# Kernel tuning notes

Hardware: AMD Instinct MI355X
Metric: run time of the kernel (lower is better)

## Reference

```python
import jax, jax.numpy as jnp
import numpy as np

S = 16   # num_states
C = 8    # input_channels
B = 64   # batch
L = 4096 # sequence length


def hyperbolic_sigmoid(x):
    return x / (1 + jnp.abs(x)) * 0.5 + 0.5


def hyperbolic_softmax(logits, axis):
    x = hyperbolic_sigmoid(logits)
    return x / jnp.sum(x, axis=axis, keepdims=True)


def setup_inputs() -> dict:
    key = jax.random.key(0)
    k0, k1, k2, k3 = jax.random.split(key, 4)
    return {
        "log_input_probs": jax.random.normal(k0, (B, L, C), dtype=jnp.float32),
        "invh_initial_state_probs": jax.random.normal(k1, (S,), dtype=jnp.float32),
        "invh_transition_probs": jax.random.normal(k2, (S, C, S), dtype=jnp.float32),
        "invh_accepting_state_probs": jax.random.normal(k3, (S,), dtype=jnp.float32),
    }


def reference(log_input_probs, invh_initial_state_probs, invh_transition_probs, invh_accepting_state_probs):
    # hyperbolic parameterization -> probabilities
    initial_state_probs = hyperbolic_softmax(invh_initial_state_probs, axis=0)         # (S,)
    transition_probs = hyperbolic_softmax(invh_transition_probs, axis=2)               # (S,C,S)
    accepting_state_logprobs = jnp.log(hyperbolic_sigmoid(invh_accepting_state_probs)) # (S,)

    input_probs = jnp.exp(log_input_probs)  # (B,L,C)
    # per-timestep transition matrices, (B,L,S,S)
    trans_each = jnp.einsum('pcn,blc->blpn', transition_probs, input_probs)
    # log-depth chain product m0 @ m1 @ ... @ m_{L-1} via associative scan
    prefix = jax.lax.associative_scan(jnp.matmul, trans_each, axis=1)
    transition_overall = prefix[:, -1]  # (B,S,S)
    # p_state[b,n] = sum_p overall[b,p,n] * init[p]
    p_state = jnp.einsum('bpn,p->bn', transition_overall, initial_state_probs)
    log_p_state = jnp.log(p_state + 1e-20)
    log_acceptance = jax.nn.logsumexp(log_p_state + accepting_state_logprobs[None, :], axis=1)  # (B,)
    return log_acceptance[None]  # (1,B)
```

## Files before the change

kernel.cpp:

```cpp
#include <hip/hip_runtime.h>
#include <math.h>

#define S 16
#define C 8
#define NB 64
#define L 4096
#define K 64
#define LC 64

#define SLOT 324
#define RS 20

typedef __attribute__((ext_vector_type(8))) short bf16x8;
typedef __attribute__((ext_vector_type(4))) short bf16x4;
typedef __attribute__((ext_vector_type(4))) float f32x4;
typedef unsigned long long ull;

#define WS_INIT 0
#define WS_ACC  64
#define WS_CLOG 512
#define WS_TTT  16896
#define WS_CP   49664

__device__ __forceinline__ float hsig(float x) {
    return x / (1.0f + fabsf(x)) * 0.5f + 0.5f;
}
__device__ __forceinline__ unsigned short f2bf(float f) {
    unsigned int u = __float_as_uint(f);
    return (unsigned short)((u + 0x7fffu + ((u >> 16) & 1u)) >> 16);
}

__device__ __forceinline__ f32x4 mfma16(bf16x4 a, bf16x4 b, f32x4 c) {
#if __has_builtin(__builtin_amdgcn_mfma_f32_16x16x16bf16_1k)
    return __builtin_amdgcn_mfma_f32_16x16x16bf16_1k(a, b, c, 0, 0, 0);
#else
    bf16x8 a8 = {a[0], a[1], a[2], a[3], 0, 0, 0, 0};
    bf16x8 b8 = {b[0], b[1], b[2], b[3], 0, 0, 0, 0};
    return __builtin_amdgcn_mfma_f32_16x16x32_bf16(a8, b8, c, 0, 0, 0);
#endif
}

__device__ __forceinline__ bf16x4 ldfrag4(const unsigned short* base, int lane) {
    return *(const bf16x4*)(base + (lane & 15) * RS + (lane >> 4) * 4);
}
__device__ __forceinline__ bf16x4 ldfrag_g4(const unsigned short* base, int lane) {
    return *(const bf16x4*)(base + (lane & 15) * 16 + (lane >> 4) * 4);
}
__device__ __forceinline__ bf16x4 cvt4(f32x4 d) {
    bf16x4 r;
    r[0] = (short)f2bf(d[0]); r[1] = (short)f2bf(d[1]);
    r[2] = (short)f2bf(d[2]); r[3] = (short)f2bf(d[3]);
    return r;
}
__device__ __forceinline__ void store16(unsigned short* slot, f32x4 d, int lane, bool odd) {
    int col = lane & 15, quad = lane >> 4;
    if (odd) {
        ull pk = (ull)f2bf(d[0]) | ((ull)f2bf(d[1]) << 16)
               | ((ull)f2bf(d[2]) << 32) | ((ull)f2bf(d[3]) << 48);
        *(ull*)(slot + col * RS + quad * 4) = pk;
    } else {
#pragma unroll
        for (int r = 0; r < 4; r++) slot[(quad * 4 + r) * RS + col] = f2bf(d[r]);
    }
}

__device__ __forceinline__ f32x4 tree_upper(unsigned short* slots, int lane, int w,
                                            bf16x4 B1a, bf16x4 B1b) {
    f32x4 z = {0.f, 0.f, 0.f, 0.f};
    f32x4 dA = mfma16(ldfrag4(slots + (8 * w) * SLOT, lane), B1a, z);
    store16(slots + (8 * w) * SLOT, dA, lane, false);
    f32x4 dB = mfma16(ldfrag4(slots + (8 * w + 4) * SLOT, lane), B1b, z);
    bf16x4 B2 = cvt4(dB);
    f32x4 d3 = mfma16(ldfrag4(slots + (8 * w) * SLOT, lane), B2, z);
    store16(slots + (8 * w) * SLOT, d3, lane, w & 1);
    __syncthreads();
    if (w < 2) {
        f32x4 d4 = mfma16(ldfrag4(slots + (16 * w) * SLOT, lane),
                          ldfrag4(slots + (16 * w + 8) * SLOT, lane), z);
        store16(slots + (16 * w) * SLOT, d4, lane, w & 1);
    }
    __syncthreads();
    return mfma16(ldfrag4(slots, lane), ldfrag4(slots + 16 * SLOT, lane), z);
}

__global__ void __launch_bounds__(256) prepall_kernel(const float* __restrict__ invh_init,
                                                      const float* __restrict__ invh_T,
                                                      const float* __restrict__ invh_acc,
                                                      unsigned char* __restrict__ wsb) {
    __shared__ float Tn[2048];
    int t = threadIdx.x;
    int cc = blockIdx.x, c = cc >> 3, c2 = cc & 7;
    if (t < S * C) {
        float v[S]; float s = 0.f;
#pragma unroll
        for (int n = 0; n < S; n++) { v[n] = hsig(invh_T[t * S + n]); s += v[n]; }
        float inv = 1.f / s;
#pragma unroll
        for (int n = 0; n < S; n++) Tn[t * S + n] = v[n] * inv;
    }
    __syncthreads();
    int p = t >> 4, n = t & 15;
    float a = 0.f;
#pragma unroll
    for (int k = 0; k < S; k++) a += Tn[(p * 8 + c) * 16 + k] * Tn[(k * 8 + c2) * 16 + n];
    ((unsigned short*)(wsb + WS_TTT))[t * 64 + cc] = f2bf(a);

    if (cc == 0 && t < S) {
        float s = 0.f;
#pragma unroll
        for (int k = 0; k < S; k++) s += hsig(invh_init[k]);
        ((float*)(wsb + WS_INIT))[t] = hsig(invh_init[t]) / s;
        ((float*)(wsb + WS_ACC))[t] = logf(hsig(invh_acc[t]));
    }
}

__global__ void __launch_bounds__(256) chunk_kernel(const float* __restrict__ logx,
                                                    unsigned char* __restrict__ wsb) {
    __shared__ __align__(16) unsigned short slots[32 * SLOT];
    __shared__ __align__(16) float xs[LC * C];
    __shared__ float clpart[4];

    int tid = threadIdx.x, lane = tid & 63, w = tid >> 6;
    int col = lane & 15, quad = lane >> 4;
    int chunk = blockIdx.x, b = blockIdx.y;

    const unsigned short* TTT = (const unsigned short*)(wsb + WS_TTT);
    bf16x8 bfr[4][2];
#pragma unroll
    for (int jj = 0; jj < 4; jj++) {
        int t = 4 * w + jj;
#pragma unroll
        for (int kk = 0; kk < 2; kk++)
            bfr[jj][kk] = *(const bf16x8*)(TTT + (t * 16 + col) * 64 + kk * 32 + quad * 8);
    }

    const float* xg = logx + ((size_t)b * L + (size_t)chunk * LC) * C;
    float2 v = *(const float2*)(xg + 2 * tid);
    float m = fmaxf(v.x, v.y);
    m = fmaxf(m, __shfl_xor(m, 1));
    m = fmaxf(m, __shfl_xor(m, 2));
    float e0 = __expf(v.x - m), e1 = __expf(v.y - m);
    float s = e0 + e1;
    s += __shfl_xor(s, 1);
    s += __shfl_xor(s, 2);
    float inv = 1.0f / s;
    *(float2*)(xs + 2 * tid) = make_float2(e0 * inv, e1 * inv);
    float lx = ((tid & 3) == 0) ? (m + __logf(s)) : 0.f;
#pragma unroll
    for (int d = 1; d < 64; d <<= 1) lx += __shfl_xor(lx, d);
    if (lane == 0) clpart[w] = lx;
    __syncthreads();
    if (tid == 0)
        ((float*)(wsb + WS_CLOG))[b * K + chunk] = clpart[0] + clpart[1] + clpart[2] + clpart[3];

    bf16x8 afr[2][2];
#pragma unroll
    for (int mt = 0; mt < 2; mt++) {
        int i2 = 2 * (mt * 16 + col);
        const float4* x1p = (const float4*)(xs + (i2 + 1) * 8);
        float4 xa = x1p[0], xb = x1p[1];
#pragma unroll
        for (int kk = 0; kk < 2; kk++) {
            float x0 = xs[i2 * 8 + kk * 4 + quad];
            bf16x8 a;
            a[0] = (short)f2bf(x0 * xa.x); a[1] = (short)f2bf(x0 * xa.y);
            a[2] = (short)f2bf(x0 * xa.z); a[3] = (short)f2bf(x0 * xa.w);
            a[4] = (short)f2bf(x0 * xb.x); a[5] = (short)f2bf(x0 * xb.y);
            a[6] = (short)f2bf(x0 * xb.z); a[7] = (short)f2bf(x0 * xb.w);
            afr[mt][kk] = a;
        }
    }

#pragma unroll
    for (int mt = 0; mt < 2; mt++)
#pragma unroll
        for (int jj = 0; jj < 4; jj++) {
            f32x4 acc = {0.f, 0.f, 0.f, 0.f};
#pragma unroll
            for (int kk = 0; kk < 2; kk++)
                acc = __builtin_amdgcn_mfma_f32_16x16x32_bf16(afr[mt][kk], bfr[jj][kk], acc, 0, 0, 0);
            int t = 4 * w + jj;
#pragma unroll
            for (int r = 0; r < 4; r++) {
                int i = mt * 16 + quad * 4 + r;
                int off = (i & 1) ? (col * RS + t) : (t * RS + col);
                slots[i * SLOT + off] = f2bf(acc[r]);
            }
        }
    __syncthreads();

    bf16x4 B1[2];
    {
        f32x4 z = {0.f, 0.f, 0.f, 0.f};
#pragma unroll
        for (int i2 = 0; i2 < 4; i2++) {
            int i = 4 * w + i2;
            f32x4 d = mfma16(ldfrag4(slots + (2 * i) * SLOT, lane),
                             ldfrag4(slots + (2 * i + 1) * SLOT, lane), z);
            if (i2 & 1) B1[i2 >> 1] = cvt4(d);
            else store16(slots + (2 * i) * SLOT, d, lane, false);
        }
    }
    f32x4 root = tree_upper(slots, lane, w, B1[0], B1[1]);

    if (w == 0) {
        unsigned short* cp = (unsigned short*)(wsb + WS_CP) + ((size_t)b * K + chunk) * 256;
        if (chunk & 1) {
            ull pk = (ull)f2bf(root[0]) | ((ull)f2bf(root[1]) << 16)
                   | ((ull)f2bf(root[2]) << 32) | ((ull)f2bf(root[3]) << 48);
            *(ull*)(cp + col * 16 + quad * 4) = pk;
        } else {
#pragma unroll
            for (int r = 0; r < 4; r++) cp[(quad * 4 + r) * 16 + col] = f2bf(root[r]);
        }
    }
}

__global__ void __launch_bounds__(256) reduce_kernel(unsigned char* __restrict__ wsb,
                                                     float* __restrict__ out) {
    __shared__ __align__(16) unsigned short slots[32 * SLOT];
    int tid = threadIdx.x, lane = tid & 63, w = tid >> 6;
    int col = lane & 15, quad = lane >> 4;
    int b = blockIdx.x;

    const unsigned short* cpb = (const unsigned short*)(wsb + WS_CP) + (size_t)b * K * 256;
    bf16x4 B0[4];
    {
        f32x4 z = {0.f, 0.f, 0.f, 0.f};
#pragma unroll
        for (int i2 = 0; i2 < 8; i2++) {
            int j = 8 * w + i2;
            f32x4 d = mfma16(ldfrag_g4(cpb + (size_t)(2 * j) * 256, lane),
                             ldfrag_g4(cpb + (size_t)(2 * j + 1) * 256, lane), z);
            if (i2 & 1) B0[i2 >> 1] = cvt4(d);
            else store16(slots + j * SLOT, d, lane, false);
        }
    }
    bf16x4 B1r[2];
    {
        f32x4 z = {0.f, 0.f, 0.f, 0.f};
#pragma unroll
        for (int i2 = 0; i2 < 4; i2++) {
            int i = 4 * w + i2;
            f32x4 d = mfma16(ldfrag4(slots + (2 * i) * SLOT, lane), B0[i2], z);
            if (i2 & 1) B1r[i2 >> 1] = cvt4(d);
            else store16(slots + (2 * i) * SLOT, d, lane, false);
        }
    }
    f32x4 troot = tree_upper(slots, lane, w, B1r[0], B1r[1]);

    if (w == 0) {
        const float* initp = (const float*)(wsb + WS_INIT);
        const float* acclog = (const float*)(wsb + WS_ACC);
        float part = 0.f;
#pragma unroll
        for (int r = 0; r < 4; r++) part += initp[quad * 4 + r] * troot[r];
        part += __shfl_xor(part, 16);
        part += __shfl_xor(part, 32);
        float lp = logf(fmaxf(part, 0.f) + 1e-30f) + acclog[col];
        float mx = lp;
#pragma unroll
        for (int d = 1; d < 16; d <<= 1) mx = fmaxf(mx, __shfl_xor(mx, d));
        float a2 = isfinite(mx) ? mx : 0.0f;
        float sm = expf(lp - a2);
#pragma unroll
        for (int d = 1; d < 16; d <<= 1) sm += __shfl_xor(sm, d);
        float cl = ((const float*)(wsb + WS_CLOG))[b * K + lane];
#pragma unroll
        for (int d = 1; d < 64; d <<= 1) cl += __shfl_xor(cl, d);
        if (lane == 0) out[b] = logf(sm) + a2 + cl;
    }
}

extern "C" void kernel_launch(void* const* d_in, const int* in_sizes, int n_in,
                              void* d_out, int out_size, void* d_ws, size_t ws_size,
                              hipStream_t stream) {
    const float* logx = (const float*)d_in[0];
    const float* init = (const float*)d_in[1];
    const float* T    = (const float*)d_in[2];
    const float* acc  = (const float*)d_in[3];
    unsigned char* wsb = (unsigned char*)d_ws;
    float* out = (float*)d_out;

    prepall_kernel<<<64, 256, 0, stream>>>(init, T, acc, wsb);
    chunk_kernel<<<dim3(K, NB), 256, 0, stream>>>(logx, wsb);
    reduce_kernel<<<NB, 256, 0, stream>>>(wsb, out);
}
```

Before: 85.41 us.

## Process two chunks per block, use packed bf16 conversion and padded xs layout

Each chunk_kernel block now handles two consecutive sequence chunks, which halves the grid and amortizes the per-block load of the TTT B-fragments. Both chunks' inputs are loaded up front. The hand-written bf16 rounding is replaced with HIP intrinsics that can convert two floats at once, and the xs staging array is padded to stride 10 to reduce LDS bank conflicts. The cost is fewer blocks (2048 instead of 4096), which means less parallelism to hide latency. There is also a potential shared-memory reuse hazard, because no barrier is visible between the end of one chunk's tree and the next chunk's slot writes.

```diff
diff --git a/kernel.cpp b/kernel.cpp
--- a/kernel.cpp
+++ b/kernel.cpp
@@ -1,4 +1,5 @@
 #include <hip/hip_runtime.h>
+#include <hip/hip_bf16.h>
 #include <math.h>
 
 #define S 16
@@ -10,6 +11,7 @@
 
 #define SLOT 324
 #define RS 20
+#define XSS 10
 
 typedef __attribute__((ext_vector_type(8))) short bf16x8;
 typedef __attribute__((ext_vector_type(4))) short bf16x4;
@@ -25,9 +27,13 @@
 __device__ __forceinline__ float hsig(float x) {
     return x / (1.0f + fabsf(x)) * 0.5f + 0.5f;
 }
+__device__ __forceinline__ unsigned int f2bf2(float a, float b) {
+    __hip_bfloat162 h = __float22bfloat162_rn(make_float2(a, b));
+    unsigned int u; __builtin_memcpy(&u, &h, 4); return u;
+}
 __device__ __forceinline__ unsigned short f2bf(float f) {
-    unsigned int u = __float_as_uint(f);
-    return (unsigned short)((u + 0x7fffu + ((u >> 16) & 1u)) >> 16);
+    __hip_bfloat16 h = __float2bfloat16(f);
+    unsigned short u; __builtin_memcpy(&u, &h, 2); return u;
 }
 
 __device__ __forceinline__ f32x4 mfma16(bf16x4 a, bf16x4 b, f32x4 c) {
@@ -47,16 +53,15 @@
     return *(const bf16x4*)(base + (lane & 15) * 16 + (lane >> 4) * 4);
 }
 __device__ __forceinline__ bf16x4 cvt4(f32x4 d) {
-    bf16x4 r;
-    r[0] = (short)f2bf(d[0]); r[1] = (short)f2bf(d[1]);
-    r[2] = (short)f2bf(d[2]); r[3] = (short)f2bf(d[3]);
-    return r;
+    union { unsigned int u[2]; bf16x4 v; } cv;
+    cv.u[0] = f2bf2(d[0], d[1]);
+    cv.u[1] = f2bf2(d[2], d[3]);
+    return cv.v;
 }
 __device__ __forceinline__ void store16(unsigned short* slot, f32x4 d, int lane, bool odd) {
     int col = lane & 15, quad = lane >> 4;
     if (odd) {
-        ull pk = (ull)f2bf(d[0]) | ((ull)f2bf(d[1]) << 16)
-               | ((ull)f2bf(d[2]) << 32) | ((ull)f2bf(d[3]) << 48);
+        ull pk = (ull)f2bf2(d[0], d[1]) | ((ull)f2bf2(d[2], d[3]) << 32);
         *(ull*)(slot + col * RS + quad * 4) = pk;
     } else {
 #pragma unroll
@@ -117,12 +122,12 @@
 __global__ void __launch_bounds__(256) chunk_kernel(const float* __restrict__ logx,
                                                     unsigned char* __restrict__ wsb) {
     __shared__ __align__(16) unsigned short slots[32 * SLOT];
-    __shared__ __align__(16) float xs[LC * C];
+    __shared__ __align__(16) float xs[LC * XSS];
     __shared__ float clpart[4];
 
     int tid = threadIdx.x, lane = tid & 63, w = tid >> 6;
     int col = lane & 15, quad = lane >> 4;
-    int chunk = blockIdx.x, b = blockIdx.y;
+    int chunk0 = 2 * blockIdx.x, b = blockIdx.y;
 
     const unsigned short* TTT = (const unsigned short*)(wsb + WS_TTT);
     bf16x8 bfr[4][2];
@@ -134,84 +139,92 @@
             bfr[jj][kk] = *(const bf16x8*)(TTT + (t * 16 + col) * 64 + kk * 32 + quad * 8);
     }
 
-    const float* xg = logx + ((size_t)b * L + (size_t)chunk * LC) * C;
-    float2 v = *(const float2*)(xg + 2 * tid);
-    float m = fmaxf(v.x, v.y);
-    m = fmaxf(m, __shfl_xor(m, 1));
-    m = fmaxf(m, __shfl_xor(m, 2));
-    float e0 = __expf(v.x - m), e1 = __expf(v.y - m);
-    float s = e0 + e1;
-    s += __shfl_xor(s, 1);
-    s += __shfl_xor(s, 2);
-    float inv = 1.0f / s;
-    *(float2*)(xs + 2 * tid) = make_float2(e0 * inv, e1 * inv);
-    float lx = ((tid & 3) == 0) ? (m + __logf(s)) : 0.f;
-#pragma unroll
-    for (int d = 1; d < 64; d <<= 1) lx += __shfl_xor(lx, d);
-    if (lane == 0) clpart[w] = lx;
-    __syncthreads();
-    if (tid == 0)
-        ((float*)(wsb + WS_CLOG))[b * K + chunk] = clpart[0] + clpart[1] + clpart[2] + clpart[3];
-
-    bf16x8 afr[2][2];
-#pragma unroll
-    for (int mt = 0; mt < 2; mt++) {
-        int i2 = 2 * (mt * 16 + col);
-        const float4* x1p = (const float4*)(xs + (i2 + 1) * 8);
-        float4 xa = x1p[0], xb = x1p[1];
-#pragma unroll
-        for (int kk = 0; kk < 2; kk++) {
-            float x0 = xs[i2 * 8 + kk * 4 + quad];
-            bf16x8 a;
-            a[0] = (short)f2bf(x0 * xa.x); a[1] = (short)f2bf(x0 * xa.y);
-            a[2] = (short)f2bf(x0 * xa.z); a[3] = (short)f2bf(x0 * xa.w);
-            a[4] = (short)f2bf(x0 * xb.x); a[5] = (short)f2bf(x0 * xb.y);
-            a[6] = (short)f2bf(x0 * xb.z); a[7] = (short)f2bf(x0 * xb.w);
-            afr[mt][kk] = a;
-        }
-    }
-
-#pragma unroll
-    for (int mt = 0; mt < 2; mt++)
-#pragma unroll
-        for (int jj = 0; jj < 4; jj++) {
-            f32x4 acc = {0.f, 0.f, 0.f, 0.f};
-#pragma unroll
-            for (int kk = 0; kk < 2; kk++)
-                acc = __builtin_amdgcn_mfma_f32_16x16x32_bf16(afr[mt][kk], bfr[jj][kk], acc, 0, 0, 0);
-            int t = 4 * w + jj;
-#pragma unroll
-            for (int r = 0; r < 4; r++) {
-                int i = mt * 16 + quad * 4 + r;
-                int off = (i & 1) ? (col * RS + t) : (t * RS + col);
-                slots[i * SLOT + off] = f2bf(acc[r]);
+    const float* xg = logx + ((size_t)b * L + (size_t)chunk0 * LC) * C;
+    float2 vv[2];
+    vv[0] = *(const float2*)(xg + 2 * tid);
+    vv[1] = *(const float2*)(xg + LC * C + 2 * tid);
+
+#pragma unroll
+    for (int ch = 0; ch < 2; ch++) {
+        int chunk = chunk0 + ch;
+
+        float2 v = vv[ch];
+        float m = fmaxf(v.x, v.y);
+        m = fmaxf(m, __shfl_xor(m, 1));
+        m = fmaxf(m, __shfl_xor(m, 2));
+        float e0 = __expf(v.x - m), e1 = __expf(v.y - m);
+        float s = e0 + e1;
+        s += __shfl_xor(s, 1);
+        s += __shfl_xor(s, 2);
+        float inv = 1.0f / s;
+        *(float2*)(xs + (tid >> 2) * XSS + 2 * (tid & 3)) = make_float2(e0 * inv, e1 * inv);
+        float lx = ((tid & 3) == 0) ? (m + __logf(s)) : 0.f;
+#pragma unroll
+        for (int d = 1; d < 64; d <<= 1) lx += __shfl_xor(lx, d);
+        if (lane == 0) clpart[w] = lx;
+        __syncthreads();
+        if (tid == 0)
+            ((float*)(wsb + WS_CLOG))[b * K + chunk] = clpart[0] + clpart[1] + clpart[2] + clpart[3];
+
+        bf16x8 afr[2][2];
+#pragma unroll
+        for (int mt = 0; mt < 2; mt++) {
+            int i2 = 2 * (mt * 16 + col);
+            const float2* x1p = (const float2*)(xs + (i2 + 1) * XSS);
+            float2 q0 = x1p[0], q1 = x1p[1], q2 = x1p[2], q3 = x1p[3];
+#pragma unroll
+            for (int kk = 0; kk < 2; kk++) {
+                float x0 = xs[i2 * XSS + kk * 4 + quad];
+                union { unsigned int u[4]; bf16x8 v8; } cv;
+                cv.u[0] = f2bf2(x0 * q0.x, x0 * q0.y);
+                cv.u[1] = f2bf2(x0 * q1.x, x0 * q1.y);
+                cv.u[2] = f2bf2(x0 * q2.x, x0 * q2.y);
+                cv.u[3] = f2bf2(x0 * q3.x, x0 * q3.y);
+                afr[mt][kk] = cv.v8;
             }
         }
-    __syncthreads();
-
-    bf16x4 B1[2];
-    {
-        f32x4 z = {0.f, 0.f, 0.f, 0.f};
-#pragma unroll
-        for (int i2 = 0; i2 < 4; i2++) {
-            int i = 4 * w + i2;
-            f32x4 d = mfma16(ldfrag4(slots + (2 * i) * SLOT, lane),
-                             ldfrag4(slots + (2 * i + 1) * SLOT, lane), z);
-            if (i2 & 1) B1[i2 >> 1] = cvt4(d);
-            else store16(slots + (2 * i) * SLOT, d, lane, false);
-        }
-    }
-    f32x4 root = tree_upper(slots, lane, w, B1[0], B1[1]);
-
-    if (w == 0) {
-        unsigned short* cp = (unsigned short*)(wsb + WS_CP) + ((size_t)b * K + chunk) * 256;
-        if (chunk & 1) {
-            ull pk = (ull)f2bf(root[0]) | ((ull)f2bf(root[1]) << 16)
-                   | ((ull)f2bf(root[2]) << 32) | ((ull)f2bf(root[3]) << 48);
-            *(ull*)(cp + col * 16 + quad * 4) = pk;
-        } else {
-#pragma unroll
-            for (int r = 0; r < 4; r++) cp[(quad * 4 + r) * 16 + col] = f2bf(root[r]);
+
+#pragma unroll
+        for (int mt = 0; mt < 2; mt++)
+#pragma unroll
+            for (int jj = 0; jj < 4; jj++) {
+                f32x4 acc = {0.f, 0.f, 0.f, 0.f};
+#pragma unroll
+                for (int kk = 0; kk < 2; kk++)
+                    acc = __builtin_amdgcn_mfma_f32_16x16x32_bf16(afr[mt][kk], bfr[jj][kk], acc, 0, 0, 0);
+                int t = 4 * w + jj;
+#pragma unroll
+                for (int r = 0; r < 4; r++) {
+                    int i = mt * 16 + quad * 4 + r;
+                    int off = (i & 1) ? (col * RS + t) : (t * RS + col);
+                    slots[i * SLOT + off] = f2bf(acc[r]);
+                }
+            }
+        __syncthreads();
+
+        bf16x4 B1[2];
+        {
+            f32x4 z = {0.f, 0.f, 0.f, 0.f};
+#pragma unroll
+            for (int i2 = 0; i2 < 4; i2++) {
+                int i = 4 * w + i2;
+                f32x4 d = mfma16(ldfrag4(slots + (2 * i) * SLOT, lane),
+                                 ldfrag4(slots + (2 * i + 1) * SLOT, lane), z);
+                if (i2 & 1) B1[i2 >> 1] = cvt4(d);
+                else store16(slots + (2 * i) * SLOT, d, lane, false);
+            }
+        }
+        f32x4 root = tree_upper(slots, lane, w, B1[0], B1[1]);
+
+        if (w == 0) {
+            unsigned short* cp = (unsigned short*)(wsb + WS_CP) + ((size_t)b * K + chunk) * 256;
+            if (chunk & 1) {
+                ull pk = (ull)f2bf2(root[0], root[1]) | ((ull)f2bf2(root[2], root[3]) << 32);
+                *(ull*)(cp + col * 16 + quad * 4) = pk;
+            } else {
+#pragma unroll
+                for (int r = 0; r < 4; r++) cp[(quad * 4 + r) * 16 + col] = f2bf(root[r]);
+            }
         }
     }
 }
@@ -283,6 +296,6 @@
     float* out = (float*)d_out;
 
     prepall_kernel<<<64, 256, 0, stream>>>(init, T, acc, wsb);
-    chunk_kernel<<<dim3(K, NB), 256, 0, stream>>>(logx, wsb);
+    chunk_kernel<<<dim3(K / 2, NB), 256, 0, stream>>>(logx, wsb);
     reduce_kernel<<<NB, 256, 0, stream>>>(wsb, out);
 }
```

New measurement: 83.66 us. -2.0%, faster.
